# Optimization experiments

Hardware: AMD Instinct MI355X
Metric: run time of the kernel (lower is better)

## Reference

```python
import jax, jax.numpy as jnp
import numpy as np

D = 1024
H = 16
K = D // H
B = 2
S = 2048

def setup_inputs() -> dict:
    key = jax.random.key(0)
    k1, k2, k3, k4, k5 = jax.random.split(key, 5)
    x = jax.random.normal(k1, (B, S, D), dtype=jnp.float32)
    # nn.Linear(d, 3d): weight [3d, d], bias [3d]
    Wqkv = jax.random.normal(k2, (3 * D, D), dtype=jnp.float32) / np.sqrt(D)
    bqkv = jax.random.normal(k3, (3 * D,), dtype=jnp.float32) * 0.01
    Wproj = jax.random.normal(k4, (D, D), dtype=jnp.float32) / np.sqrt(D)
    bproj = jax.random.normal(k5, (D,), dtype=jnp.float32) * 0.01
    return {"x": x, "Wqkv": Wqkv, "bqkv": bqkv, "Wproj": Wproj, "bproj": bproj}

def reference(x, Wqkv, bqkv, Wproj, bproj):
    Bsz, Slen, d = x.shape
    # fused QKV projection: [B,S,3d] -> [B,S,3,H,K] -> (3, B, H, S, K)
    qkv = (jnp.einsum('bsd,ed->bse', x, Wqkv) + bqkv).reshape(Bsz, Slen, 3, H, K)
    q, k, v = jnp.moveaxis(qkv, 2, 0).transpose(0, 1, 3, 2, 4)
    scale = 1.0 / jnp.sqrt(jnp.asarray(K, dtype=x.dtype))
    scores = jnp.einsum('bhqk,bhmk->bhqm', q, k) * scale  # [B,H,S,S]
    a = jax.nn.softmax(scores, axis=-1)
    # dropout is identity in eval mode
    o = jnp.einsum('bhqm,bhmk->bhqk', a, v)  # [B,H,S,K]
    o = o.transpose(0, 2, 1, 3).reshape(Bsz, Slen, d)
    return jnp.einsum('bsd,ed->bse', o, Wproj) + bproj
```

## Files before the change

kernel.cpp:

```cpp
#include <hip/hip_runtime.h>
#include <cstdint>

typedef unsigned short ushort_t;
typedef short short8 __attribute__((ext_vector_type(8)));
typedef float f32x4 __attribute__((ext_vector_type(4)));
typedef float float4v __attribute__((ext_vector_type(4)));
typedef unsigned int uint2v __attribute__((ext_vector_type(2)));
typedef unsigned int uint4v __attribute__((ext_vector_type(4)));

#define DDIM 1024
#define HH 16
#define HEADK 64
#define BB 2
#define SS 2048

#if __has_builtin(__builtin_amdgcn_exp2f)
#define EXP2F(x) __builtin_amdgcn_exp2f(x)
#else
#define EXP2F(x) exp2f(x)
#endif

__device__ __forceinline__ ushort_t f2bf(float f) {
  union { float f; uint32_t u; } c; c.f = f;
  uint32_t u = c.u;
  u += 0x7fffu + ((u >> 16) & 1u);
  return (ushort_t)(u >> 16);
}

__device__ __forceinline__ uint32_t pkbf_trunc(float a, float b) {
  union { float f; uint32_t u; } ca, cb;
  ca.f = a; cb.f = b;
  return __builtin_amdgcn_perm(cb.u, ca.u, 0x07060302);
}

__device__ __forceinline__ uint32_t pkbf_rne(float a, float b) {
  return (uint32_t)f2bf(a) | ((uint32_t)f2bf(b) << 16);
}

__device__ __forceinline__ float bfhi2f(uint32_t u) {
  union { uint32_t u; float f; } c; c.u = u & 0xffff0000u; return c.f;
}
__device__ __forceinline__ float bflo2f(uint32_t u) {
  union { uint32_t u; float f; } c; c.u = u << 16; return c.f;
}

__device__ __forceinline__ void glds16(const ushort_t* gp, ushort_t* lp) {
  __builtin_amdgcn_global_load_lds(
      (const __attribute__((address_space(1))) uint32_t*)gp,
      (__attribute__((address_space(3))) uint32_t*)lp, 16, 0, 0);
}

__global__ void cvt3_kernel(const float* __restrict__ s0, ushort_t* __restrict__ d0, int n0,
                            const float* __restrict__ s1, ushort_t* __restrict__ d1, int n1,
                            const float* __restrict__ s2, ushort_t* __restrict__ d2, int n2) {
  int i = blockIdx.x * blockDim.x + threadIdx.x;
  const float* src; ushort_t* dst; int k;
  if (i < n0) { src = s0; dst = d0; k = i; }
  else if (i < n0 + n1) { src = s1; dst = d1; k = i - n0; }
  else if (i < n0 + n1 + n2) { src = s2; dst = d2; k = i - n0 - n1; }
  else return;
  float4v v = ((const float4v*)src)[k];
  uint2v o; o[0] = pkbf_rne(v[0], v[1]); o[1] = pkbf_rne(v[2], v[3]);
  ((uint2v*)dst)[k] = o;
}

__global__ __launch_bounds__(256) void gemm_qkv128(
    const ushort_t* __restrict__ A, const ushort_t* __restrict__ Bm,
    const float* __restrict__ bias, ushort_t* __restrict__ Cbf) {
  constexpr int Kd = 1024;
  __shared__ ushort_t smem[128 * 64 * 2];
  ushort_t* As = smem;
  ushort_t* Bs = smem + 128 * 64;
  const int tid = threadIdx.x;
  const int wv = tid >> 6, lane = tid & 63;
  const int l15 = lane & 15, quad = lane >> 4;
  const int wm = wv >> 1, wn = wv & 1;

  const int lin = blockIdx.x + 24 * blockIdx.y;
  const int xcd = lin & 7, g = lin >> 3;
  const int by = xcd + 8 * (g & 3);
  const int bx = g >> 2;
  const int tm0 = by * 128, tn0 = bx * 128;

  f32x4 acc[4][4];
#pragma unroll
  for (int i = 0; i < 4; ++i)
#pragma unroll
    for (int j = 0; j < 4; ++j) acc[i][j] = (f32x4){0.f, 0.f, 0.f, 0.f};

  const int lrow = lane >> 3;
  const int gcb = (lane & 7) ^ lrow;

  for (int k0 = 0; k0 < Kd; k0 += 64) {
#pragma unroll
    for (int c = 0; c < 4; ++c) {
      int seg = wv * 4 + c;
      glds16(A + (size_t)(tm0 + seg * 8 + lrow) * Kd + k0 + gcb * 8,
             As + seg * 512);
    }
#pragma unroll
    for (int c = 0; c < 4; ++c) {
      int seg = wv * 4 + c;
      glds16(Bm + (size_t)(tn0 + seg * 8 + lrow) * Kd + k0 + gcb * 8,
             Bs + seg * 512);
    }
    __syncthreads();
#pragma unroll
    for (int kk = 0; kk < 64; kk += 32) {
      short8 af[4], bfr[4];
#pragma unroll
      for (int i = 0; i < 4; ++i) {
        int r = wm * 64 + i * 16 + l15;
        int cb = (kk >> 3) + quad;
        af[i] = *(const short8*)(As + r * 64 + ((cb ^ (l15 & 7)) << 3));
      }
#pragma unroll
      for (int j = 0; j < 4; ++j) {
        int r = wn * 64 + j * 16 + l15;
        int cb = (kk >> 3) + quad;
        bfr[j] = *(const short8*)(Bs + r * 64 + ((cb ^ (l15 & 7)) << 3));
      }
#pragma unroll
      for (int i = 0; i < 4; ++i)
#pragma unroll
        for (int j = 0; j < 4; ++j)
          acc[i][j] = __builtin_amdgcn_mfma_f32_16x16x32_bf16(
              af[i], bfr[j], acc[i][j], 0, 0, 0);
    }
    __syncthreads();
  }

  const int t = tn0 >> 10;
  if (t < 2) {
#pragma unroll
    for (int j = 0; j < 4; ++j) {
      int col = tn0 + wn * 64 + j * 16 + l15;
      float bv = bias[col];
      int hh = (col >> 6) & 15, kk2 = col & 63;
#pragma unroll
      for (int i = 0; i < 4; ++i) {
        int row0 = tm0 + wm * 64 + i * 16 + quad * 4;
#pragma unroll
        for (int r = 0; r < 4; ++r) {
          int row = row0 + r;
          int b = row >> 11, s = row & 2047;
          float v = acc[i][j][r] + bv;
          if (t == 0) v *= 0.18033688f;
          size_t base = (((size_t)t * BB + b) * HH + hh) * ((size_t)SS * HEADK);
          Cbf[base + (size_t)s * HEADK + kk2] = f2bf(v);
        }
      }
    }
  } else {
    __syncthreads();
#pragma unroll
    for (int j = 0; j < 4; ++j) {
      int c = wn * 64 + j * 16 + l15;
      float bv = bias[tn0 + c];
#pragma unroll
      for (int i = 0; i < 4; ++i) {
        int row0 = wm * 64 + i * 16 + quad * 4;
        uint2v dw;
        dw[0] = pkbf_rne(acc[i][j][0] + bv, acc[i][j][1] + bv);
        dw[1] = pkbf_rne(acc[i][j][2] + bv, acc[i][j][3] + bv);
        int rb = row0 >> 3;
        *(uint2v*)(&smem[c * 128 + (((rb ^ (c & 15)) << 3) | (row0 & 7))]) = dw;
      }
    }
    __syncthreads();
    const int rb2 = lane & 15;
    const int cg = lane >> 4;
#pragma unroll
    for (int it = 0; it < 8; ++it) {
      int c = wv * 32 + it * 4 + cg;
      short8 vv = *(const short8*)(&smem[c * 128 + ((rb2 ^ (c & 15)) << 3)]);
      int gcol = tn0 + c;
      int hh = (gcol >> 6) & 15, kk2 = gcol & 63;
      int grow = tm0 + rb2 * 8;
      int b = grow >> 11, s = grow & 2047;
      size_t base = (((size_t)2 * BB + b) * HH + hh) * ((size_t)SS * HEADK);
      *(short8*)(&Cbf[base + (size_t)kk2 * SS + s]) = vv;
    }
  }
}

__global__ __launch_bounds__(256, 2) void gemm_proj(
    const ushort_t* __restrict__ Op0, const ushort_t* __restrict__ Op1,
    const float* __restrict__ Lp, const ushort_t* __restrict__ Bm,
    const float* __restrict__ bias, float* __restrict__ Cout) {
  constexpr int Kd = 1024;
  constexpr size_t nsL = (size_t)BB * HH * SS;
  __shared__ ushort_t smem[2 * 12288];
  const int tid = threadIdx.x;
  const int wv = tid >> 6, lane = tid & 63;
  const int l15 = lane & 15, quad = lane >> 4;
  const int wm = wv >> 1, wn = wv & 1;
  const int lrow = lane >> 3, gcb = (lane & 7) ^ lrow;

  const int lin = blockIdx.x + 16 * blockIdx.y;
  const int xcd = lin & 7, g = lin >> 3;
  const int by = xcd + 8 * (g & 3);
  const int bx = g >> 2;
  const int tm0 = by * 128, tn0 = bx * 64;

  f32x4 acc[4][2];
#pragma unroll
  for (int i = 0; i < 4; ++i)
#pragma unroll
    for (int j = 0; j < 2; ++j) acc[i][j] = (f32x4){0.f, 0.f, 0.f, 0.f};

  struct ARegs {
    uint4v ra0[2], ra1[2], rb0[2], rb1[2];
    float rl0[2], rl1[2];
  };
  ARegs sA, sB;

  auto readA = [&](int t, ARegs& S) {
#pragma unroll
    for (int c = 0; c < 2; ++c) {
      int u = tid + 256 * c;
      int row = u >> 2, cg = u & 3;
      int grw = tm0 + row;
      int ab = grw >> 11, as_ = grw & 2047;
      size_t lo = (size_t)(ab * HH + t) * SS + as_;
      size_t po = lo * 64 + cg * 16;
      S.ra0[c] = *(const uint4v*)(Op0 + po);
      S.ra1[c] = *(const uint4v*)(Op0 + po + 8);
      S.rb0[c] = *(const uint4v*)(Op1 + po);
      S.rb1[c] = *(const uint4v*)(Op1 + po + 8);
      S.rl0[c] = Lp[lo];
      S.rl1[c] = Lp[nsL + lo];
    }
  };
  auto writeA = [&](const ARegs& S, int pp) {
    ushort_t* As = smem + pp * 12288;
#pragma unroll
    for (int c = 0; c < 2; ++c) {
      int u = tid + 256 * c;
      int row = u >> 2, cg = u & 3;
      float inv = 1.0f / (S.rl0[c] + S.rl1[c]);
      uint4v olo, ohi;
#pragma unroll
      for (int d = 0; d < 4; ++d) {
        olo[d] = pkbf_rne((bflo2f(S.ra0[c][d]) + bflo2f(S.rb0[c][d])) * inv,
                          (bfhi2f(S.ra0[c][d]) + bfhi2f(S.rb0[c][d])) * inv);
        ohi[d] = pkbf_rne((bflo2f(S.ra1[c][d]) + bflo2f(S.rb1[c][d])) * inv,
                          (bfhi2f(S.ra1[c][d]) + bfhi2f(S.rb1[c][d])) * inv);
      }
      *(uint4v*)(&As[row * 64 + (((cg * 2) ^ (row & 7)) << 3)]) = olo;
      *(uint4v*)(&As[row * 64 + (((cg * 2 + 1) ^ (row & 7)) << 3)]) = ohi;
    }
  };
  auto stageB = [&](int t, int pp) {
    ushort_t* Bs = smem + pp * 12288 + 8192;
#pragma unroll
    for (int c = 0; c < 2; ++c) {
      int seg = wv * 2 + c;
      glds16(Bm + (size_t)(tn0 + seg * 8 + lrow) * Kd + t * 64 + gcb * 8,
             Bs + seg * 512);
    }
  };

  readA(0, sA);
  __builtin_amdgcn_sched_barrier(0);
  stageB(0, 0);
  __builtin_amdgcn_sched_barrier(0);
  readA(1, sB);
  __builtin_amdgcn_sched_barrier(0);
  asm volatile("s_waitcnt vmcnt(14)" ::: "memory");
  writeA(sA, 0);
  asm volatile("s_waitcnt lgkmcnt(0)" ::: "memory");
  asm volatile("s_waitcnt vmcnt(12)" ::: "memory");
  __builtin_amdgcn_s_barrier();
  __builtin_amdgcn_sched_barrier(0);

#pragma unroll
  for (int t = 0; t < 16; ++t) {
    const int p = t & 1;
    if (t + 1 < 16) {
      stageB(t + 1, p ^ 1);
      __builtin_amdgcn_sched_barrier(0);
    }
    if (t + 2 < 16) {
      if (t & 1) readA(t + 2, sB); else readA(t + 2, sA);
      __builtin_amdgcn_sched_barrier(0);
    }

    const ushort_t* As = smem + p * 12288;
    const ushort_t* Bs = As + 8192;
    short8 bfr[2][2], af[4][2];
#pragma unroll
    for (int j = 0; j < 2; ++j)
#pragma unroll
      for (int kc = 0; kc < 2; ++kc) {
        int n = wn * 32 + j * 16 + l15;
        bfr[j][kc] =
            *(const short8*)(Bs + n * 64 + (((kc * 4 + quad) ^ (l15 & 7)) << 3));
      }
#pragma unroll
    for (int mi = 0; mi < 4; ++mi)
#pragma unroll
      for (int kc = 0; kc < 2; ++kc) {
        int r = wm * 64 + mi * 16 + l15;
        af[mi][kc] =
            *(const short8*)(As + r * 64 + (((kc * 4 + quad) ^ (l15 & 7)) << 3));
      }
    __builtin_amdgcn_s_setprio(1);
#pragma unroll
    for (int kc = 0; kc < 2; ++kc)
#pragma unroll
      for (int mi = 0; mi < 4; ++mi)
#pragma unroll
        for (int j = 0; j < 2; ++j)
          acc[mi][j] = __builtin_amdgcn_mfma_f32_16x16x32_bf16(
              af[mi][kc], bfr[j][kc], acc[mi][j], 0, 0, 0);
    __builtin_amdgcn_s_setprio(0);

    if (t + 1 < 16) {
      if (t < 14)
        asm volatile("s_waitcnt vmcnt(14)" ::: "memory");
      else
        asm volatile("s_waitcnt vmcnt(2)" ::: "memory");
      if (t & 1) writeA(sA, p ^ 1); else writeA(sB, p ^ 1);
      asm volatile("s_waitcnt lgkmcnt(0)" ::: "memory");
      if (t < 14)
        asm volatile("s_waitcnt vmcnt(12)" ::: "memory");
      else
        asm volatile("s_waitcnt vmcnt(0)" ::: "memory");
      __builtin_amdgcn_s_barrier();
      __builtin_amdgcn_sched_barrier(0);
    }
  }

#pragma unroll
  for (int j = 0; j < 2; ++j) {
    int col = tn0 + wn * 32 + j * 16 + l15;
    float bv = bias[col];
#pragma unroll
    for (int mi = 0; mi < 4; ++mi) {
      int row0 = tm0 + wm * 64 + mi * 16 + quad * 4;
#pragma unroll
      for (int r = 0; r < 4; ++r)
        Cout[(size_t)(row0 + r) * 1024 + col] = acc[mi][j][r] + bv;
    }
  }
}

template <int NSPLIT>
__global__ __launch_bounds__(256, 4) void attn_kernel(
    const ushort_t* __restrict__ qkv, ushort_t* __restrict__ O0,
    ushort_t* __restrict__ O1, float* __restrict__ Lp) {
  constexpr int NT = (SS / NSPLIT) / 32;
  __shared__ ushort_t Kt[3][32 * 64];
  __shared__ ushort_t Vt[3][64 * 32];
  __shared__ ushort_t Pw[4][2][32 * 32];

  const int lin = blockIdx.x + 16 * (blockIdx.y + 16 * blockIdx.z);
  const int xcd = lin & 7, ii = lin >> 3;
  const int qt = ii & 15;
  const int hz = (ii >> 4) * 8 + xcd;
  const int h = hz & 15;
  const int z = hz >> 4;
  const int b = z >> 1, ns = z & 1;
  const int tid = threadIdx.x;
  const int wv = tid >> 6, lane = tid & 63;
  const int l15 = lane & 15, quad = lane >> 4;

  const size_t hstride = (size_t)SS * HEADK;
  const ushort_t* Qg = qkv + ((size_t)(0 * BB + b) * HH + h) * hstride;
  const ushort_t* Kg = qkv + ((size_t)(1 * BB + b) * HH + h) * hstride;
  const ushort_t* Vg = qkv + ((size_t)(2 * BB + b) * HH + h) * hstride;
  ushort_t* Opp = ns ? O1 : O0;

  short8 qf[2][2];
#pragma unroll
  for (int mi = 0; mi < 2; ++mi)
#pragma unroll
    for (int kc = 0; kc < 2; ++kc)
      qf[mi][kc] = *(const short8*)(
          Qg + (size_t)(qt * 128 + wv * 32 + mi * 16 + l15) * 64 + kc * 32 +
          quad * 8);

  const short ONE = (short)0x3F80;
  short8 ones = {ONE, ONE, ONE, ONE, ONE, ONE, ONE, ONE};

  f32x4 oat[2][4];
  f32x4 loa[2];
#pragma unroll
  for (int mi = 0; mi < 2; ++mi) {
    loa[mi] = (f32x4){0.f, 0.f, 0.f, 0.f};
#pragma unroll
    for (int c = 0; c < 4; ++c) oat[mi][c] = (f32x4){0.f, 0.f, 0.f, 0.f};
  }

  const int lrow = lane >> 3, gcb = (lane & 7) ^ lrow;
  const int vfl = lane >> 2;
  const int vgb = (lane & 3) ^ ((vfl >> 1) & 3);

  const int pos0 = ns * (SS / NSPLIT);

  auto stage = [&](int jj, int db) {
    glds16(Kg + (size_t)(pos0 + jj * 32 + wv * 8 + lrow) * 64 + gcb * 8,
           &Kt[db][wv * 512]);
    glds16(Vg + (size_t)(wv * 16 + vfl) * SS + pos0 + jj * 32 + vgb * 8,
           &Vt[db][wv * 512]);
  };

  auto qk_phase = [&](int kb, int pb) {
    f32x4 st[2][2];
    __builtin_amdgcn_s_setprio(1);
#pragma unroll
    for (int cf = 0; cf < 2; ++cf) {
      int n = cf * 16 + l15;
      short8 kf0 = *(const short8*)(&Kt[kb][n * 64 + ((quad ^ (n & 7)) << 3)]);
      short8 kf1 =
          *(const short8*)(&Kt[kb][n * 64 + (((quad + 4) ^ (n & 7)) << 3)]);
#pragma unroll
      for (int mi = 0; mi < 2; ++mi) {
        f32x4 z2 = (f32x4){0.f, 0.f, 0.f, 0.f};
        z2 = __builtin_amdgcn_mfma_f32_16x16x32_bf16(kf0, qf[mi][0], z2, 0, 0, 0);
        z2 = __builtin_amdgcn_mfma_f32_16x16x32_bf16(kf1, qf[mi][1], z2, 0, 0, 0);
        st[mi][cf] = z2;
      }
    }
    __builtin_amdgcn_s_setprio(0);
#pragma unroll
    for (int mi = 0; mi < 2; ++mi)
#pragma unroll
      for (int cf = 0; cf < 2; ++cf) {
        float e0 = EXP2F(st[mi][cf][0]);
        float e1 = EXP2F(st[mi][cf][1]);
        float e2 = EXP2F(st[mi][cf][2]);
        float e3 = EXP2F(st[mi][cf][3]);
        uint2v dw;
        dw[0] = pkbf_trunc(e0, e1);
        dw[1] = pkbf_trunc(e2, e3);
        int row = mi * 16 + l15;
        int pbv = 2 * cf + (quad >> 1);
        int pbs = pbv ^ ((l15 >> 1) & 3);
        *(uint2v*)(&Pw[wv][pb][row * 32 + pbs * 8 + (quad & 1) * 4]) = dw;
      }
  };

  stage(0, 0);
  stage(1, 1);

  asm volatile("s_waitcnt vmcnt(2)" ::: "memory");
  __builtin_amdgcn_s_barrier();
  asm volatile("" ::: "memory");
  __builtin_amdgcn_sched_barrier(0);
  qk_phase(0, 0);

  int vb = 0;
  for (int j = 0; j < NT; ++j) {
    const int kb = (vb == 2) ? 0 : vb + 1;
    const int sb = (kb == 2) ? 0 : kb + 1;
    asm volatile("s_waitcnt vmcnt(0)" ::: "memory");
    __builtin_amdgcn_s_barrier();
    asm volatile("" ::: "memory");
    __builtin_amdgcn_sched_barrier(0);

    if (j + 2 < NT) stage(j + 2, sb);
    if (j + 1 < NT) qk_phase(kb, (j + 1) & 1);

    short8 pa[2];
#pragma unroll
    for (int mi = 0; mi < 2; ++mi) {
      int row = mi * 16 + l15;
      pa[mi] = *(const short8*)(&Pw[wv][j & 1][row * 32 +
                                              ((quad ^ ((l15 >> 1) & 3)) << 3)]);
    }
    __builtin_amdgcn_s_setprio(1);
#pragma unroll
    for (int cf = 0; cf < 4; ++cf) {
      short8 vf = *(const short8*)(&Vt[vb][(cf * 16 + l15) * 32 +
                                           ((quad ^ ((l15 >> 1) & 3)) << 3)]);
#pragma unroll
      for (int mi = 0; mi < 2; ++mi)
        oat[mi][cf] = __builtin_amdgcn_mfma_f32_16x16x32_bf16(
            vf, pa[mi], oat[mi][cf], 0, 0, 0);
    }
#pragma unroll
    for (int mi = 0; mi < 2; ++mi)
      loa[mi] = __builtin_amdgcn_mfma_f32_16x16x32_bf16(ones, pa[mi], loa[mi],
                                                        0, 0, 0);
    __builtin_amdgcn_s_setprio(0);

    vb = kb;
  }

  const size_t obase = ((size_t)b * HH + h) * SS * HEADK;
#pragma unroll
  for (int mi = 0; mi < 2; ++mi) {
#pragma unroll
    for (int cf = 0; cf < 4; ++cf) {
      uint2v dw;
      dw[0] = pkbf_rne(oat[mi][cf][0], oat[mi][cf][1]);
      dw[1] = pkbf_rne(oat[mi][cf][2], oat[mi][cf][3]);
      int cb = 2 * cf + (quad >> 1);
      int cbs = cb ^ (l15 & 7);
      *(uint2v*)(&Pw[wv][0][l15 * 64 + cbs * 8 + (quad & 1) * 4]) = dw;
    }
    const int r = lane >> 2;
#pragma unroll
    for (int pass = 0; pass < 2; ++pass) {
      int g = (lane & 3) + 4 * pass;
      short8 ov = *(const short8*)(&Pw[wv][0][r * 64 + ((g ^ (r & 7)) << 3)]);
      int qrow = qt * 128 + wv * 32 + mi * 16 + r;
      *(short8*)(&Opp[obase + (size_t)qrow * 64 + g * 8]) = ov;
    }
    if (quad == 0) {
      int qrow = qt * 128 + wv * 32 + mi * 16 + l15;
      Lp[((size_t)(ns * BB + b) * HH + h) * SS + qrow] = loa[mi][0];
    }
  }
}

extern "C" void kernel_launch(void* const* d_in, const int* in_sizes, int n_in,
                              void* d_out, int out_size, void* d_ws,
                              size_t ws_size, hipStream_t stream) {
  const float* x = (const float*)d_in[0];
  const float* Wqkv = (const float*)d_in[1];
  const float* bqkv = (const float*)d_in[2];
  const float* Wproj = (const float*)d_in[3];
  const float* bproj = (const float*)d_in[4];
  float* out = (float*)d_out;

  ushort_t* xb = (ushort_t*)d_ws;
  ushort_t* wqb = xb + (size_t)4096 * 1024;
  ushort_t* wpb = wqb + (size_t)3072 * 1024;
  ushort_t* qkvb = wpb + (size_t)1024 * 1024;
  ushort_t* Op1 = qkvb + (size_t)3 * BB * HH * SS * HEADK;
  ushort_t* Op0 = xb;
  float* Lp = (float*)wqb;

  const int n0 = 4096 * 1024 / 4, n1 = 3072 * 1024 / 4, n2 = 1024 * 1024 / 4;
  cvt3_kernel<<<(n0 + n1 + n2 + 255) / 256, 256, 0, stream>>>(
      x, xb, n0, Wqkv, wqb, n1, Wproj, wpb, n2);
  gemm_qkv128<<<dim3(3072 / 128, 4096 / 128), 256, 0, stream>>>(xb, wqb, bqkv,
                                                                qkvb);
  attn_kernel<2><<<dim3(16, 16, 4), 256, 0, stream>>>(qkvb, Op0, Op1, Lp);
  gemm_proj<<<dim3(1024 / 64, 4096 / 128), 256, 0, stream>>>(
      Op0, Op1, Lp, wpb, bproj, out);
}
```

Baseline: 192.9 us.

## Load K/V fragments directly from global into registers, drop LDS staging

Replaces the LDS triple-buffered K/V staging (global-to-LDS copies plus block barriers) with per-wave direct global loads of K and V MFMA fragments into registers. K is double-buffered in registers and prefetched two tiles ahead, and the loop is unrolled by two. This removes LDS traffic and the per-iteration block barrier. In exchange each wave redundantly fetches the same K/V tile from global/L2, and V loads are strided by the sequence length. It also raises register pressure under launch_bounds(256,4).

```diff
diff --git a/kernel.cpp b/kernel.cpp
--- a/kernel.cpp
+++ b/kernel.cpp
@@ -351,8 +351,6 @@
     const ushort_t* __restrict__ qkv, ushort_t* __restrict__ O0,
     ushort_t* __restrict__ O1, float* __restrict__ Lp) {
   constexpr int NT = (SS / NSPLIT) / 32;
-  __shared__ ushort_t Kt[3][32 * 64];
-  __shared__ ushort_t Vt[3][64 * 32];
   __shared__ ushort_t Pw[4][2][32 * 32];
 
   const int lin = blockIdx.x + 16 * (blockIdx.y + 16 * blockIdx.z);
@@ -393,36 +391,43 @@
     for (int c = 0; c < 4; ++c) oat[mi][c] = (f32x4){0.f, 0.f, 0.f, 0.f};
   }
 
-  const int lrow = lane >> 3, gcb = (lane & 7) ^ lrow;
-  const int vfl = lane >> 2;
-  const int vgb = (lane & 3) ^ ((vfl >> 1) & 3);
-
   const int pos0 = ns * (SS / NSPLIT);
-
-  auto stage = [&](int jj, int db) {
-    glds16(Kg + (size_t)(pos0 + jj * 32 + wv * 8 + lrow) * 64 + gcb * 8,
-           &Kt[db][wv * 512]);
-    glds16(Vg + (size_t)(wv * 16 + vfl) * SS + pos0 + jj * 32 + vgb * 8,
-           &Vt[db][wv * 512]);
-  };
-
-  auto qk_phase = [&](int kb, int pb) {
+  const ushort_t* Kbase = Kg + (size_t)pos0 * 64;
+  const ushort_t* Vbase = Vg + pos0;
+
+  struct KSet { short8 k[2][2]; };
+  struct VSet { short8 v[4]; };
+
+  auto loadK = [&](int j, KSet& S) {
+#pragma unroll
+    for (int cf = 0; cf < 2; ++cf) {
+      const ushort_t* p =
+          Kbase + (size_t)(j * 32 + cf * 16 + l15) * 64 + quad * 8;
+      S.k[cf][0] = *(const short8*)(p);
+      S.k[cf][1] = *(const short8*)(p + 32);
+    }
+  };
+  auto loadV = [&](int j, VSet& S) {
+#pragma unroll
+    for (int cf = 0; cf < 4; ++cf)
+      S.v[cf] = *(const short8*)(Vbase + (size_t)(cf * 16 + l15) * SS +
+                                 j * 32 + quad * 8);
+  };
+
+  auto qk_phase = [&](const KSet& S, int pb) {
     f32x4 st[2][2];
     __builtin_amdgcn_s_setprio(1);
 #pragma unroll
-    for (int cf = 0; cf < 2; ++cf) {
-      int n = cf * 16 + l15;
-      short8 kf0 = *(const short8*)(&Kt[kb][n * 64 + ((quad ^ (n & 7)) << 3)]);
-      short8 kf1 =
-          *(const short8*)(&Kt[kb][n * 64 + (((quad + 4) ^ (n & 7)) << 3)]);
+    for (int cf = 0; cf < 2; ++cf)
 #pragma unroll
       for (int mi = 0; mi < 2; ++mi) {
         f32x4 z2 = (f32x4){0.f, 0.f, 0.f, 0.f};
-        z2 = __builtin_amdgcn_mfma_f32_16x16x32_bf16(kf0, qf[mi][0], z2, 0, 0, 0);
-        z2 = __builtin_amdgcn_mfma_f32_16x16x32_bf16(kf1, qf[mi][1], z2, 0, 0, 0);
+        z2 = __builtin_amdgcn_mfma_f32_16x16x32_bf16(S.k[cf][0], qf[mi][0], z2,
+                                                     0, 0, 0);
+        z2 = __builtin_amdgcn_mfma_f32_16x16x32_bf16(S.k[cf][1], qf[mi][1], z2,
+                                                     0, 0, 0);
         st[mi][cf] = z2;
       }
-    }
     __builtin_amdgcn_s_setprio(0);
 #pragma unroll
     for (int mi = 0; mi < 2; ++mi)
@@ -442,27 +447,7 @@
       }
   };
 
-  stage(0, 0);
-  stage(1, 1);
-
-  asm volatile("s_waitcnt vmcnt(2)" ::: "memory");
-  __builtin_amdgcn_s_barrier();
-  asm volatile("" ::: "memory");
-  __builtin_amdgcn_sched_barrier(0);
-  qk_phase(0, 0);
-
-  int vb = 0;
-  for (int j = 0; j < NT; ++j) {
-    const int kb = (vb == 2) ? 0 : vb + 1;
-    const int sb = (kb == 2) ? 0 : kb + 1;
-    asm volatile("s_waitcnt vmcnt(0)" ::: "memory");
-    __builtin_amdgcn_s_barrier();
-    asm volatile("" ::: "memory");
-    __builtin_amdgcn_sched_barrier(0);
-
-    if (j + 2 < NT) stage(j + 2, sb);
-    if (j + 1 < NT) qk_phase(kb, (j + 1) & 1);
-
+  auto pv_phase = [&](const VSet& S, int j) {
     short8 pa[2];
 #pragma unroll
     for (int mi = 0; mi < 2; ++mi) {
@@ -472,21 +457,45 @@
     }
     __builtin_amdgcn_s_setprio(1);
 #pragma unroll
-    for (int cf = 0; cf < 4; ++cf) {
-      short8 vf = *(const short8*)(&Vt[vb][(cf * 16 + l15) * 32 +
-                                           ((quad ^ ((l15 >> 1) & 3)) << 3)]);
+    for (int cf = 0; cf < 4; ++cf)
 #pragma unroll
       for (int mi = 0; mi < 2; ++mi)
         oat[mi][cf] = __builtin_amdgcn_mfma_f32_16x16x32_bf16(
-            vf, pa[mi], oat[mi][cf], 0, 0, 0);
-    }
+            S.v[cf], pa[mi], oat[mi][cf], 0, 0, 0);
 #pragma unroll
     for (int mi = 0; mi < 2; ++mi)
       loa[mi] = __builtin_amdgcn_mfma_f32_16x16x32_bf16(ones, pa[mi], loa[mi],
                                                         0, 0, 0);
     __builtin_amdgcn_s_setprio(0);
-
-    vb = kb;
+  };
+
+  KSet k0, k1;
+  VSet vv;
+
+  loadK(0, k0);
+  qk_phase(k0, 0);
+  loadK(1, k1);
+
+#pragma unroll 1
+  for (int jj = 0; jj < NT / 2; ++jj) {
+    {
+      const int j = 2 * jj;
+      loadV(j, vv);
+      int jn = (j + 2 < NT) ? (j + 2) : (NT - 1);
+      loadK(jn, k0);
+      __builtin_amdgcn_sched_barrier(0);
+      qk_phase(k1, (j + 1) & 1);
+      pv_phase(vv, j);
+    }
+    {
+      const int j = 2 * jj + 1;
+      loadV(j, vv);
+      int jn = (j + 2 < NT) ? (j + 2) : (NT - 1);
+      loadK(jn, k1);
+      __builtin_amdgcn_sched_barrier(0);
+      if (j + 1 < NT) qk_phase(k0, (j + 1) & 1);
+      pv_phase(vv, j);
+    }
   }
 
   const size_t obase = ((size_t)b * HH + h) * SS * HEADK;
```

Result: slower. 271.8 us (+40.9%).
